# Optimization experiments

Hardware: AMD Instinct MI355X
Metric: run time of the kernel (lower is better)

The kernel has to match this reference:

```python
import jax, jax.numpy as jnp
import numpy as np

B, H, W, C = 8, 64, 64, 256
CF = C // 8  # f/g projection channels


def setup_inputs() -> dict:
    key = jax.random.key(0)
    ks = jax.random.split(key, 7)
    glorot = lambda k, shape, fan_in, fan_out: jax.random.uniform(
        k, shape, jnp.float32, -1.0, 1.0) * np.sqrt(6.0 / (fan_in + fan_out))
    return {
        "x": jax.random.normal(ks[0], (B, H, W, C), jnp.float32),
        "kernel_f": glorot(ks[1], (1, 1, C, CF), C, CF),
        "kernel_g": glorot(ks[2], (1, 1, C, CF), C, CF),
        "kernel_h": glorot(ks[3], (1, 1, C, C), C, C),
        "bias_f": jnp.zeros((CF,), jnp.float32),
        "bias_g": jnp.zeros((CF,), jnp.float32),
        "bias_h": jnp.zeros((C,), jnp.float32),
        "gamma": jnp.zeros((1,), jnp.float32),
    }


def reference(x, kernel_f, kernel_g, kernel_h, bias_f, bias_g, bias_h, gamma):
    b, h, w, c = x.shape
    n = h * w
    xf = x.reshape(b, n, c)  # hw_flatten; 1x1 conv == per-pixel GEMM
    f = jnp.einsum('bnc,cd->bnd', xf, kernel_f[0, 0]) + bias_f  # [B,N,C/8]
    g = jnp.einsum('bnc,cd->bnd', xf, kernel_g[0, 0]) + bias_g  # [B,N,C/8]
    hh = jnp.einsum('bnc,cd->bnd', xf, kernel_h[0, 0]) + bias_h  # [B,N,C]
    s = jnp.einsum('bid,bjd->bij', g, f)  # matmul(g, f^T): [B,N,N]
    beta = jax.nn.softmax(s, axis=-1)
    o = jnp.einsum('bij,bjc->bic', beta, hh)  # [B,N,C]
    return gamma * o.reshape(b, h, w, c) + x
```

## Files before the change

### kernel.cpp

```cpp
#include <hip/hip_runtime.h>
#include <hip/hip_bf16.h>

#define BATCH 8
#define NTOK 4096
#define CH 256
#define CF 32
#define KVBLK 128
#define NITER (NTOK / KVBLK)

typedef float v4f __attribute__((ext_vector_type(4)));
typedef float v16f __attribute__((ext_vector_type(16)));
typedef short v8s __attribute__((ext_vector_type(8)));

static __device__ __forceinline__ ushort f2bf(float f) {
    union { float f; uint u; } v; v.f = f;
    uint u = v.u;
    uint r = (u + 0x7fffu + ((u >> 16) & 1u)) >> 16;
    return (ushort)r;
}

static __device__ __forceinline__ uint cvt_pk(float lo, float hi) {
    uint r;
    asm("v_cvt_pk_bf16_f32 %0, %1, %2" : "=v"(r) : "v"(lo), "v"(hi));
    return r;
}

static __device__ __forceinline__ void plswap(uint& a, uint& b) {
    asm("v_permlane32_swap_b32 %0, %1" : "+v"(a), "+v"(b));
}

static __device__ __forceinline__ void gload16(const void* g, void* l) {
    __builtin_amdgcn_global_load_lds(
        (const __attribute__((address_space(1))) unsigned int*)g,
        (__attribute__((address_space(3))) unsigned int*)l, 16, 0, 0);
}

#define MFMA16(a, b, c) __builtin_amdgcn_mfma_f32_16x16x32_bf16(a, b, c, 0, 0, 0)
#define MFMA32(a, b, c) __builtin_amdgcn_mfma_f32_32x32x16_bf16(a, b, c, 0, 0, 0)

__global__ __launch_bounds__(256) void prep_weights(
    const float* __restrict__ kf, const float* __restrict__ kg,
    const float* __restrict__ kh,
    ushort* __restrict__ wfT, ushort* __restrict__ wgT, ushort* __restrict__ whT) {
    __shared__ float tile[64][33];
    int bid = blockIdx.x;
    const float* src; ushort* dst; int cols, k0, c0;
    if (bid < 32)      { src = kh; dst = whT; cols = 256; k0 = (bid >> 3) * 64; c0 = (bid & 7) * 32; }
    else if (bid < 36) { src = kf; dst = wfT; cols = 32;  k0 = (bid - 32) * 64; c0 = 0; }
    else               { src = kg; dst = wgT; cols = 32;  k0 = (bid - 36) * 64; c0 = 0; }
    int t = threadIdx.x;
    int kr = t >> 2, cb = (t & 3) * 8;
#pragma unroll
    for (int j = 0; j < 8; ++j) tile[kr][cb + j] = src[(size_t)(k0 + kr) * cols + c0 + cb + j];
    __syncthreads();
    int c = t >> 3, kc = (t & 7) * 8;
    ushort tmp[8];
#pragma unroll
    for (int j = 0; j < 8; ++j) tmp[j] = f2bf(tile[kc + j][c]);
    *(uint4*)(dst + (size_t)(c0 + c) * CH + k0 + kc) = *(uint4*)tmp;
}

__global__ __launch_bounds__(256) void proj_fgx(
    const float* __restrict__ x, const ushort* __restrict__ wfT,
    const ushort* __restrict__ wgT, const float* __restrict__ bf,
    const float* __restrict__ bg,
    ushort* __restrict__ fo, ushort* __restrict__ go, ushort* __restrict__ XT) {
    __shared__ __align__(16) ushort xl[64 * 256];
    __shared__ __align__(16) ushort wl[2][32 * 256];
    int tid = threadIdx.x;
    int lane = tid & 63, w = tid >> 6;
    int row15 = lane & 15, g4 = lane >> 4;
    int n0 = blockIdx.x * 64;
    int batch = n0 >> 12, nn0 = n0 & (NTOK - 1);

#pragma unroll
    for (int i = 0; i < 8; ++i) {
        int id = i * 256 + tid;
        int sel = id >> 10, r = (id >> 5) & 31, s = id & 31;
        const ushort* src = (sel ? wgT : wfT) + r * CH + ((s ^ (r & 7)) << 3);
        gload16(src, (char*)&wl[0][0] + id * 16);
    }
#pragma unroll
    for (int i = 0; i < 8; ++i) {
        int id = i * 256 + tid;
        int n = id >> 5, cc = id & 31;
        const float* xp = x + (size_t)(n0 + n) * CH + cc * 8;
        float4 a0 = ((const float4*)xp)[0], a1 = ((const float4*)xp)[1];
        uint4 pv;
        pv.x = cvt_pk(a0.x, a0.y); pv.y = cvt_pk(a0.z, a0.w);
        pv.z = cvt_pk(a1.x, a1.y); pv.w = cvt_pk(a1.z, a1.w);
        *(uint4*)((char*)xl + n * 512 + ((cc ^ (n & 7)) << 4)) = pv;
    }
    asm volatile("s_waitcnt vmcnt(0)" ::: "memory");
    __syncthreads();

    v4f accF[2] = {}, accG[2] = {};
    int nrow = w * 16 + row15;
    for (int ks = 0; ks < 8; ++ks) {
        v8s xf = *(const v8s*)((char*)xl + nrow * 512 + (((ks * 4 + g4) ^ (nrow & 7)) << 4));
#pragma unroll
        for (int ct = 0; ct < 2; ++ct) {
            int wr = ct * 16 + row15;
            int wb = wr * 512 + (((ks * 4 + g4) ^ (wr & 7)) << 4);
            v8s bwf = *(const v8s*)((char*)&wl[0][0] + wb);
            v8s bwg = *(const v8s*)((char*)&wl[1][0] + wb);
            accF[ct] = MFMA16(xf, bwf, accF[ct]);
            accG[ct] = MFMA16(xf, bwg, accG[ct]);
        }
    }
#pragma unroll
    for (int ct = 0; ct < 2; ++ct)
#pragma unroll
        for (int r = 0; r < 4; ++r) {
            int n = n0 + w * 16 + g4 * 4 + r;
            int cf = ct * 16 + row15;
            fo[(size_t)n * CF + cf] = f2bf(accF[ct][r] + bf[cf]);
            go[(size_t)n * CF + cf] = f2bf(accG[ct][r] + bg[cf]);
        }

    ushort* XTb = XT + (size_t)batch * CH * NTOK;
    int c = tid;
#pragma unroll
    for (int i = 0; i < 8; ++i) {
        ushort tmp[8];
#pragma unroll
        for (int j = 0; j < 8; ++j) {
            int row = i * 8 + j;
            int chunk = (c >> 3) ^ j;
            tmp[j] = xl[row * 256 + chunk * 8 + (c & 7)];
        }
        *(uint4*)(XTb + (size_t)c * NTOK + nn0 + i * 8) = *(uint4*)tmp;
    }
}

__global__ __launch_bounds__(512, 1) void flash_attn(
    const ushort* __restrict__ fbuf, const ushort* __restrict__ gbuf,
    const ushort* __restrict__ XT,
    ushort* __restrict__ PX, float* __restrict__ lsw) {
    __shared__ __align__(16) ushort lds_v[2][32768];
    __shared__ float lsx[4][32];

    int tid = threadIdx.x;
    int lane = tid & 63, w = tid >> 6;
    int row31 = lane & 31, h = lane >> 5;
    int batch = blockIdx.x & 7;
    int qg = w >> 1, kh = w & 1;
    int q0 = (blockIdx.x >> 3) * 128 + qg * 32;

    const ushort* fB = fbuf + (size_t)batch * NTOK * CF;
    const ushort* gB = gbuf + (size_t)batch * NTOK * CF;
    const ushort* vB = XT + (size_t)batch * CH * NTOK;

    int crow = tid >> 4;
    int koffe = ((tid & 15) ^ (crow & 15)) << 3;
    const ushort* vpb = vB + (size_t)crow * NTOK + koffe;

#define STAGE(buf) do {                                                    \
        _Pragma("unroll")                                                  \
        for (int i_ = 0; i_ < 8; ++i_)                                     \
            gload16(vpb + (size_t)(i_ * 32) * NTOK,                        \
                    (char*)&lds_v[buf][0] + (i_ * 512 + tid) * 16);        \
    } while (0)

    const ushort* kp = fB + (size_t)(kh * 64 + row31) * CF + h * 8;

    int voff[2][2];
#pragma unroll
    for (int kt = 0; kt < 2; ++kt)
#pragma unroll
        for (int j = 0; j < 2; ++j) {
            int ch = kh * 8 + (kt * 2 + j) * 2 + h;
            voff[kt][j] = row31 * 256 + ((ch ^ (row31 & 15)) << 4);
        }

    v8s bq[2];
    bq[0] = *(const v8s*)(gB + (size_t)(q0 + row31) * CF + h * 8);
    bq[1] = *(const v8s*)(gB + (size_t)(q0 + row31) * CF + 16 + h * 8);

    float lsum = 0.f;
    v16f acc[8] = {};
    const v16f z16 = {};

    v8s k00 = *(const v8s*)kp;
    v8s k01 = *(const v8s*)(kp + 16);
    v8s k10 = *(const v8s*)(kp + 32 * CF);
    v8s k11 = *(const v8s*)(kp + 32 * CF + 16);
    kp += KVBLK * CF;
    STAGE(0); vpb += KVBLK;

    for (int t = 0; t < NITER; ++t) {
        int cur = t & 1;
        __builtin_amdgcn_s_barrier();
        v8s n00 = {}, n01 = {}, n10 = {}, n11 = {};
        if (t + 1 < NITER) {
            STAGE(cur ^ 1); vpb += KVBLK;
            n00 = *(const v8s*)kp;
            n01 = *(const v8s*)(kp + 16);
            n10 = *(const v8s*)(kp + 32 * CF);
            n11 = *(const v8s*)(kp + 32 * CF + 16);
            kp += KVBLK * CF;
            asm volatile("s_waitcnt vmcnt(12)" ::: "memory");
        } else {
            asm volatile("s_waitcnt vmcnt(0)" ::: "memory");
        }
        __builtin_amdgcn_s_barrier();

        const char* vb = (const char*)&lds_v[cur][0];

        v16f s0, s1;
        s0 = MFMA32(k00, bq[0], z16); s0 = MFMA32(k01, bq[1], s0);
        s1 = MFMA32(k10, bq[0], z16); s1 = MFMA32(k11, bq[1], s1);

        float psum = 0.f;
#pragma unroll
        for (int r = 0; r < 16; ++r) {
            s0[r] = __builtin_amdgcn_exp2f(s0[r] * 1.44269504f - 34.6246924f);
            s1[r] = __builtin_amdgcn_exp2f(s1[r] * 1.44269504f - 34.6246924f);
            psum += s0[r] + s1[r];
        }
        lsum += psum;

        __builtin_amdgcn_s_setprio(1);
#pragma unroll
        for (int kt = 0; kt < 2; ++kt)
#pragma unroll
            for (int j = 0; j < 2; ++j) {
                int R = j * 8;
                uint a0, a1, b0, b1;
                if (kt == 0) {
                    a0 = cvt_pk(s0[R + 0], s0[R + 1]); a1 = cvt_pk(s0[R + 2], s0[R + 3]);
                    b0 = cvt_pk(s0[R + 4], s0[R + 5]); b1 = cvt_pk(s0[R + 6], s0[R + 7]);
                } else {
                    a0 = cvt_pk(s1[R + 0], s1[R + 1]); a1 = cvt_pk(s1[R + 2], s1[R + 3]);
                    b0 = cvt_pk(s1[R + 4], s1[R + 5]); b1 = cvt_pk(s1[R + 6], s1[R + 7]);
                }
                plswap(a0, b0);
                plswap(a1, b1);
                union { v8s v; uint u[4]; } pu;
                pu.u[0] = a0; pu.u[1] = a1; pu.u[2] = b0; pu.u[3] = b1;
#pragma unroll
                for (int ct = 0; ct < 8; ++ct) {
                    v8s bv = *(const v8s*)(vb + voff[kt][j] + ct * 8192);
                    acc[ct] = MFMA32(pu.v, bv, acc[ct]);
                }
            }
        __builtin_amdgcn_s_setprio(0);
        k00 = n00; k01 = n01; k10 = n10; k11 = n11;
    }
#undef STAGE

    lsum += __shfl_xor(lsum, 32);

    float* mbuf = (float*)&lds_v[0][0];
    int p = qg;
    if (kh == 1) {
        lsx[p][row31] = lsum;
#pragma unroll
        for (int ct = 0; ct < 4; ++ct)
#pragma unroll
            for (int r = 0; r < 16; ++r) {
                int qrow = (r & 3) + 8 * (r >> 2) + 4 * h;
                mbuf[p * 4096 + qrow * 128 + ct * 32 + row31] = acc[ct][r];
            }
    }
    __syncthreads();
    if (kh == 0) {
        float ltot = lsum + lsx[p][row31];
        if (h == 0) lsw[batch * NTOK + q0 + row31] = ltot;
#pragma unroll
        for (int ct = 0; ct < 4; ++ct)
#pragma unroll
            for (int r = 0; r < 16; ++r) {
                int qrow = (r & 3) + 8 * (r >> 2) + 4 * h;
                float val = acc[ct][r] + mbuf[p * 4096 + qrow * 128 + ct * 32 + row31];
                PX[((size_t)batch * NTOK + q0 + qrow) * CH + ct * 32 + row31] = f2bf(val);
            }
    }
    __syncthreads();
    if (kh == 1) {
#pragma unroll
        for (int ct = 4; ct < 8; ++ct)
#pragma unroll
            for (int r = 0; r < 16; ++r) {
                int qrow = (r & 3) + 8 * (r >> 2) + 4 * h;
                mbuf[p * 4096 + qrow * 128 + (ct - 4) * 32 + row31] = acc[ct][r];
            }
    }
    __syncthreads();
    if (kh == 0) {
#pragma unroll
        for (int ct = 4; ct < 8; ++ct)
#pragma unroll
            for (int r = 0; r < 16; ++r) {
                int qrow = (r & 3) + 8 * (r >> 2) + 4 * h;
                float val = acc[ct][r] + mbuf[p * 4096 + qrow * 128 + (ct - 4) * 32 + row31];
                PX[((size_t)batch * NTOK + q0 + qrow) * CH + ct * 32 + row31] = f2bf(val);
            }
    }
}

__global__ __launch_bounds__(256) void gemm_h(
    const ushort* __restrict__ PX, const ushort* __restrict__ whT,
    const float* __restrict__ lsw, const float* __restrict__ bh,
    const float* __restrict__ x, const float* __restrict__ gamma,
    float* __restrict__ out) {
    __shared__ __align__(16) ushort pxl[64 * 256];
    __shared__ __align__(16) ushort wll[64 * 256];
    int tid = threadIdx.x;
    int lane = tid & 63, w = tid >> 6;
    int row15 = lane & 15, g4 = lane >> 4;
    int n0 = blockIdx.x * 64, c0 = blockIdx.y * 64;

#pragma unroll
    for (int i = 0; i < 8; ++i) {
        int id = i * 256 + tid;
        int n = id >> 5, s = id & 31;
        gload16(PX + (size_t)(n0 + n) * CH + ((s ^ (n & 7)) << 3),
                (char*)pxl + id * 16);
    }
#pragma unroll
    for (int i = 0; i < 8; ++i) {
        int id = i * 256 + tid;
        int c = id >> 5, s = id & 31;
        gload16(whT + (size_t)(c0 + c) * CH + ((s ^ (c & 7)) << 3),
                (char*)wll + id * 16);
    }
    asm volatile("s_waitcnt vmcnt(0)" ::: "memory");
    __syncthreads();

    v4f acc[4] = {};
    int wr = w * 16 + row15;
    for (int ks = 0; ks < 8; ++ks) {
        v8s bw = *(const v8s*)((char*)wll + wr * 512 + (((ks * 4 + g4) ^ (wr & 7)) << 4));
#pragma unroll
        for (int nt = 0; nt < 4; ++nt) {
            int nr = nt * 16 + row15;
            v8s af = *(const v8s*)((char*)pxl + nr * 512 + (((ks * 4 + g4) ^ (nr & 7)) << 4));
            acc[nt] = MFMA16(af, bw, acc[nt]);
        }
    }

    float gm = gamma[0];
    int c = c0 + w * 16 + row15;
    float bhc = gm * bh[c];
#pragma unroll
    for (int nt = 0; nt < 4; ++nt)
#pragma unroll
        for (int r = 0; r < 4; ++r) {
            int n = n0 + nt * 16 + g4 * 4 + r;
            float li = 1.0f / lsw[n];
            size_t idx = (size_t)n * CH + c;
            out[idx] = gm * acc[nt][r] * li + bhc + x[idx];
        }
}

extern "C" void kernel_launch(void* const* d_in, const int* in_sizes, int n_in,
                              void* d_out, int out_size, void* d_ws, size_t ws_size,
                              hipStream_t stream) {
    const float* x  = (const float*)d_in[0];
    const float* kf = (const float*)d_in[1];
    const float* kg = (const float*)d_in[2];
    const float* kh = (const float*)d_in[3];
    const float* bf = (const float*)d_in[4];
    const float* bg = (const float*)d_in[5];
    const float* bh = (const float*)d_in[6];
    const float* gm = (const float*)d_in[7];
    float* out = (float*)d_out;

    char* ws = (char*)d_ws;
    ushort* wfT = (ushort*)(ws);
    ushort* wgT = (ushort*)(ws + 16384);
    ushort* whT = (ushort*)(ws + 32768);
    ushort* fo  = (ushort*)(ws + 163840);
    ushort* go  = (ushort*)(ws + 163840 + 2097152);
    ushort* XT  = (ushort*)(ws + 4358144);
    ushort* PX  = (ushort*)(ws + 4358144 + 16777216);
    float*  lsw = (float* )(ws + 4358144 + 33554432);

    hipLaunchKernelGGL(prep_weights, dim3(40), dim3(256), 0, stream, kf, kg, kh, wfT, wgT, whT);
    hipLaunchKernelGGL(proj_fgx, dim3(512), dim3(256), 0, stream,
                       x, wfT, wgT, bf, bg, fo, go, XT);
    hipLaunchKernelGGL(flash_attn, dim3(256), dim3(512), 0, stream, fo, go, XT, PX, lsw);
    hipLaunchKernelGGL(gemm_h, dim3(512, 4), dim3(256), 0, stream,
                       PX, whT, lsw, bh, x, gm, out);
}
```

Before: 124.6 us.

## Fuse output projection GEMM into flash attention epilogue

The separate gemm_h kernel is removed. Each flash_attn block now stages its bf16 P·X tile into LDS, loads the W_h weights in two 128-channel halves, and runs the 256x256 projection with MFMA before writing the final gamma-scaled residual output. This drops the PX and row-sum round trips through global memory and one kernel launch. In exchange the attention kernel's tail grows and adds extra barriers, and with only 256 blocks at one block per CU the epilogue runs with low parallelism.

```diff
diff --git a/kernel.cpp b/kernel.cpp
--- a/kernel.cpp
+++ b/kernel.cpp
@@ -135,10 +135,12 @@
 
 __global__ __launch_bounds__(512, 1) void flash_attn(
     const ushort* __restrict__ fbuf, const ushort* __restrict__ gbuf,
-    const ushort* __restrict__ XT,
-    ushort* __restrict__ PX, float* __restrict__ lsw) {
+    const ushort* __restrict__ XT, const ushort* __restrict__ whT,
+    const float* __restrict__ x, const float* __restrict__ bh,
+    const float* __restrict__ gamma, float* __restrict__ out) {
     __shared__ __align__(16) ushort lds_v[2][32768];
     __shared__ float lsx[4][32];
+    __shared__ float lsq[128];
 
     int tid = threadIdx.x;
     int lane = tid & 63, w = tid >> 6;
@@ -251,107 +253,79 @@
 
     lsum += __shfl_xor(lsum, 32);
 
+    __syncthreads();
     float* mbuf = (float*)&lds_v[0][0];
-    int p = qg;
-    if (kh == 1) {
-        lsx[p][row31] = lsum;
-#pragma unroll
-        for (int ct = 0; ct < 4; ++ct)
-#pragma unroll
-            for (int r = 0; r < 16; ++r) {
-                int qrow = (r & 3) + 8 * (r >> 2) + 4 * h;
-                mbuf[p * 4096 + qrow * 128 + ct * 32 + row31] = acc[ct][r];
-            }
-    }
-    __syncthreads();
-    if (kh == 0) {
-        float ltot = lsum + lsx[p][row31];
-        if (h == 0) lsw[batch * NTOK + q0 + row31] = ltot;
-#pragma unroll
-        for (int ct = 0; ct < 4; ++ct)
-#pragma unroll
-            for (int r = 0; r < 16; ++r) {
-                int qrow = (r & 3) + 8 * (r >> 2) + 4 * h;
-                float val = acc[ct][r] + mbuf[p * 4096 + qrow * 128 + ct * 32 + row31];
-                PX[((size_t)batch * NTOK + q0 + qrow) * CH + ct * 32 + row31] = f2bf(val);
-            }
-    }
-    __syncthreads();
-    if (kh == 1) {
-#pragma unroll
-        for (int ct = 4; ct < 8; ++ct)
-#pragma unroll
-            for (int r = 0; r < 16; ++r) {
-                int qrow = (r & 3) + 8 * (r >> 2) + 4 * h;
-                mbuf[p * 4096 + qrow * 128 + (ct - 4) * 32 + row31] = acc[ct][r];
-            }
-    }
-    __syncthreads();
-    if (kh == 0) {
-#pragma unroll
-        for (int ct = 4; ct < 8; ++ct)
-#pragma unroll
-            for (int r = 0; r < 16; ++r) {
-                int qrow = (r & 3) + 8 * (r >> 2) + 4 * h;
-                float val = acc[ct][r] + mbuf[p * 4096 + qrow * 128 + (ct - 4) * 32 + row31];
-                PX[((size_t)batch * NTOK + q0 + qrow) * CH + ct * 32 + row31] = f2bf(val);
-            }
-    }
-}
-
-__global__ __launch_bounds__(256) void gemm_h(
-    const ushort* __restrict__ PX, const ushort* __restrict__ whT,
-    const float* __restrict__ lsw, const float* __restrict__ bh,
-    const float* __restrict__ x, const float* __restrict__ gamma,
-    float* __restrict__ out) {
-    __shared__ __align__(16) ushort pxl[64 * 256];
-    __shared__ __align__(16) ushort wll[64 * 256];
-    int tid = threadIdx.x;
-    int lane = tid & 63, w = tid >> 6;
-    int row15 = lane & 15, g4 = lane >> 4;
-    int n0 = blockIdx.x * 64, c0 = blockIdx.y * 64;
-
-#pragma unroll
-    for (int i = 0; i < 8; ++i) {
-        int id = i * 256 + tid;
-        int n = id >> 5, s = id & 31;
-        gload16(PX + (size_t)(n0 + n) * CH + ((s ^ (n & 7)) << 3),
-                (char*)pxl + id * 16);
-    }
-#pragma unroll
-    for (int i = 0; i < 8; ++i) {
-        int id = i * 256 + tid;
-        int c = id >> 5, s = id & 31;
-        gload16(whT + (size_t)(c0 + c) * CH + ((s ^ (c & 7)) << 3),
-                (char*)wll + id * 16);
-    }
-    asm volatile("s_waitcnt vmcnt(0)" ::: "memory");
-    __syncthreads();
-
-    v4f acc[4] = {};
-    int wr = w * 16 + row15;
-    for (int ks = 0; ks < 8; ++ks) {
-        v8s bw = *(const v8s*)((char*)wll + wr * 512 + (((ks * 4 + g4) ^ (wr & 7)) << 4));
-#pragma unroll
-        for (int nt = 0; nt < 4; ++nt) {
-            int nr = nt * 16 + row15;
-            v8s af = *(const v8s*)((char*)pxl + nr * 512 + (((ks * 4 + g4) ^ (nr & 7)) << 4));
-            acc[nt] = MFMA16(af, bw, acc[nt]);
-        }
+    ushort* pxt = &lds_v[1][0];
+#pragma unroll
+    for (int rd = 0; rd < 2; ++rd) {
+        if (kh == 1) {
+            if (rd == 0) lsx[qg][row31] = lsum;
+#pragma unroll
+            for (int ct = 0; ct < 4; ++ct)
+#pragma unroll
+                for (int r = 0; r < 16; ++r) {
+                    int qrow = (r & 3) + 8 * (r >> 2) + 4 * h;
+                    mbuf[qg * 4096 + qrow * 128 + ct * 32 + row31] = acc[rd * 4 + ct][r];
+                }
+        }
+        __syncthreads();
+        if (kh == 0) {
+            float ltot = lsum + lsx[qg][row31];
+            if (rd == 0 && h == 0) lsq[qg * 32 + row31] = ltot;
+#pragma unroll
+            for (int ct = 0; ct < 4; ++ct)
+#pragma unroll
+                for (int r = 0; r < 16; ++r) {
+                    int qrow = (r & 3) + 8 * (r >> 2) + 4 * h;
+                    float val = acc[rd * 4 + ct][r] + mbuf[qg * 4096 + qrow * 128 + ct * 32 + row31];
+                    int ql = qg * 32 + qrow;
+                    int c = rd * 128 + ct * 32 + row31;
+                    int cc = c >> 3;
+                    pxt[ql * 256 + (((cc ^ (ql & 15)) << 3) | (c & 7))] = f2bf(val);
+                }
+        }
+        __syncthreads();
     }
 
     float gm = gamma[0];
-    int c = c0 + w * 16 + row15;
-    float bhc = gm * bh[c];
-#pragma unroll
-    for (int nt = 0; nt < 4; ++nt)
-#pragma unroll
-        for (int r = 0; r < 4; ++r) {
-            int n = n0 + nt * 16 + g4 * 4 + r;
-            float li = 1.0f / lsw[n];
-            size_t idx = (size_t)n * CH + c;
-            out[idx] = gm * acc[nt][r] * li + bhc + x[idx];
-        }
+    const char* pb = (const char*)pxt;
+    for (int chh = 0; chh < 2; ++chh) {
+#pragma unroll
+        for (int i = 0; i < 8; ++i) {
+            int id = i * 512 + tid;
+            int c = id >> 5, s = id & 31;
+            gload16(whT + (size_t)(chh * 128 + c) * CH + ((s ^ (c & 15)) << 3),
+                    (char*)mbuf + id * 16);
+        }
+        asm volatile("s_waitcnt vmcnt(0)" ::: "memory");
+        __syncthreads();
+
+        const char* wb = (const char*)mbuf;
+        int ql = qg * 32 + row31;
+        int cl0 = kh * 64 + row31;
+        int cl1 = kh * 64 + 32 + row31;
+        v16f o0 = z16, o1 = z16;
+#pragma unroll
+        for (int ks = 0; ks < 16; ++ks) {
+            int cc = ks * 2 + h;
+            v8s a  = *(const v8s*)(pb + ql * 512 + ((cc ^ (ql & 15)) << 4));
+            v8s b0 = *(const v8s*)(wb + cl0 * 512 + ((cc ^ (cl0 & 15)) << 4));
+            v8s b1 = *(const v8s*)(wb + cl1 * 512 + ((cc ^ (cl1 & 15)) << 4));
+            o0 = MFMA32(a, b0, o0);
+            o1 = MFMA32(a, b1, o1);
+        }
+#pragma unroll
+        for (int r = 0; r < 16; ++r) {
+            int qrow = (r & 3) + 8 * (r >> 2) + 4 * h;
+            float li = gm / lsq[qg * 32 + qrow];
+            size_t nglob = (size_t)batch * NTOK + q0 + qrow;
+            int c0a = chh * 128 + kh * 64 + row31;
+            size_t i0 = nglob * CH + c0a;
+            out[i0]      = o0[r] * li + gm * bh[c0a]      + x[i0];
+            out[i0 + 32] = o1[r] * li + gm * bh[c0a + 32] + x[i0 + 32];
+        }
+        __syncthreads();
+    }
 }
 
 extern "C" void kernel_launch(void* const* d_in, const int* in_sizes, int n_in,
@@ -374,13 +348,10 @@
     ushort* fo  = (ushort*)(ws + 163840);
     ushort* go  = (ushort*)(ws + 163840 + 2097152);
     ushort* XT  = (ushort*)(ws + 4358144);
-    ushort* PX  = (ushort*)(ws + 4358144 + 16777216);
-    float*  lsw = (float* )(ws + 4358144 + 33554432);
 
     hipLaunchKernelGGL(prep_weights, dim3(40), dim3(256), 0, stream, kf, kg, kh, wfT, wgT, whT);
     hipLaunchKernelGGL(proj_fgx, dim3(512), dim3(256), 0, stream,
                        x, wfT, wgT, bf, bg, fo, go, XT);
-    hipLaunchKernelGGL(flash_attn, dim3(256), dim3(512), 0, stream, fo, go, XT, PX, lsw);
-    hipLaunchKernelGGL(gemm_h, dim3(512, 4), dim3(256), 0, stream,
-                       PX, whT, lsw, bh, x, gm, out);
-}
+    hipLaunchKernelGGL(flash_attn, dim3(256), dim3(512), 0, stream,
+                       fo, go, XT, whT, x, bh, gm, out);
+}
```

After: 122.7 us, median of 2. Within noise of the previous version (-1.6%).
